# Performance work log

Measured on AMD Instinct MI355X. Metric: run time of the kernel, lower is better.

## Reference

```python
import jax, jax.numpy as jnp
import numpy as np

MAP_SIZE = 56
K_STEEP = 10.0  # boxcar sigmoid steepness (the 'k=10' default in the original)


def setup_inputs() -> dict:
    key = jax.random.key(0)
    k1, k2, k3 = jax.random.split(key, 3)
    B, D, H = 16384, 1024, 512
    x = jax.random.normal(k1, (B, D), dtype=jnp.float32)
    W1 = jax.random.normal(k2, (D, H), dtype=jnp.float32) * (1.0 / np.sqrt(D))
    b1 = jnp.zeros((H,), dtype=jnp.float32)
    W2 = jax.random.normal(k3, (H, 3), dtype=jnp.float32) * (1.0 / np.sqrt(H))
    b2 = jnp.zeros((3,), dtype=jnp.float32)
    return {"x": x, "W1": W1, "b1": b1, "W2": W2, "b2": b2}


def boxcar(t, map_size=MAP_SIZE, k=K_STEEP):
    # t: [B, 3] = (x_center, y_center, size). Vectorized over batch and grid.
    t0 = t[:, 0][:, None, None]  # [B,1,1]
    t1 = t[:, 1][:, None, None]
    t2 = t[:, 2][:, None, None]
    i = jnp.arange(map_size, dtype=t.dtype)[None, :, None]  # [1,S,1]
    j = jnp.arange(map_size, dtype=t.dtype)[None, None, :]  # [1,1,S]
    Vx = jax.nn.sigmoid(k * (i - t0 + 0.5 * t2)) - jax.nn.sigmoid(k * (i - t0 - 0.5 * t2))
    Vy = jax.nn.sigmoid(k * (j - t1 + 0.5 * t2)) - jax.nn.sigmoid(k * (j - t1 - 0.5 * t2))
    return Vx * Vy  # [B,S,S]


def reference(x, W1, b1, W2, b2):
    # fc1 -> fc2 (flatten output is discarded in the original call(), as in source)
    h = x @ W1 + b1          # [B, hidden]
    t = h @ W2 + b2          # [B, 3]
    return boxcar(t)         # [B, map_size, map_size]
```

## Files before the change

kernel.cpp:

```cpp
#include <hip/hip_runtime.h>
#include <math.h>

#define MAP 56
#define KST 10.0f
#define BATCH 16384
#define DIM 1024
#define HID 512
#define RPB 8

typedef float floatx4 __attribute__((ext_vector_type(4)));

__global__ __launch_bounds__(64) void fold_weights(
    const float* __restrict__ W1, const float* __restrict__ b1,
    const float* __restrict__ W2, const float* __restrict__ b2,
    float* __restrict__ WeffT, float* __restrict__ beff)
{
    const int d = blockIdx.x;
    const int lane = threadIdx.x;
    const float* row = (d < DIM) ? (W1 + (size_t)d * HID) : b1;

    float a0 = 0.f, a1 = 0.f, a2 = 0.f;
    for (int h = lane; h < HID; h += 64) {
        const float w = row[h];
        a0 += w * W2[h * 3 + 0];
        a1 += w * W2[h * 3 + 1];
        a2 += w * W2[h * 3 + 2];
    }
    #pragma unroll
    for (int off = 32; off; off >>= 1) {
        a0 += __shfl_down(a0, off, 64);
        a1 += __shfl_down(a1, off, 64);
        a2 += __shfl_down(a2, off, 64);
    }
    if (lane == 0) {
        if (d < DIM) {
            WeffT[0 * DIM + d] = a0;
            WeffT[1 * DIM + d] = a1;
            WeffT[2 * DIM + d] = a2;
        } else {
            beff[0] = a0 + b2[0];
            beff[1] = a1 + b2[1];
            beff[2] = a2 + b2[2];
        }
    }
}

__global__ __launch_bounds__(256) void fused_kernel(
    const float* __restrict__ x, const float* __restrict__ WeffT,
    const float* __restrict__ beff, float* __restrict__ out)
{
    __shared__ float   sVx[RPB][MAP];
    __shared__ floatx4 sVy4[RPB][MAP / 4];
    __shared__ float   st[RPB][4];

    const int tid  = threadIdx.x;
    const int wave = tid >> 6;
    const int lane = tid & 63;
    const int base = blockIdx.x * RPB;

    const float* xr0 = x + (size_t)(base + 2 * wave + 0) * DIM + 4 * lane;
    const float* xr1 = x + (size_t)(base + 2 * wave + 1) * DIM + 4 * lane;
    float a00 = 0.f, a01 = 0.f, a02 = 0.f;
    float a10 = 0.f, a11 = 0.f, a12 = 0.f;
    #pragma unroll
    for (int q = 0; q < 4; ++q) {
        const int off = 256 * q;
        const floatx4 w0 = *(const floatx4*)(WeffT + 0 * DIM + 4 * lane + off);
        const floatx4 w1 = *(const floatx4*)(WeffT + 1 * DIM + 4 * lane + off);
        const floatx4 w2 = *(const floatx4*)(WeffT + 2 * DIM + 4 * lane + off);
        const floatx4 x0 = __builtin_nontemporal_load((const floatx4*)(xr0 + off));
        const floatx4 x1 = __builtin_nontemporal_load((const floatx4*)(xr1 + off));
        a00 += x0.x * w0.x + x0.y * w0.y + x0.z * w0.z + x0.w * w0.w;
        a01 += x0.x * w1.x + x0.y * w1.y + x0.z * w1.z + x0.w * w1.w;
        a02 += x0.x * w2.x + x0.y * w2.y + x0.z * w2.z + x0.w * w2.w;
        a10 += x1.x * w0.x + x1.y * w0.y + x1.z * w0.z + x1.w * w0.w;
        a11 += x1.x * w1.x + x1.y * w1.y + x1.z * w1.z + x1.w * w1.w;
        a12 += x1.x * w2.x + x1.y * w2.y + x1.z * w2.z + x1.w * w2.w;
    }
    #pragma unroll
    for (int off = 32; off; off >>= 1) {
        a00 += __shfl_down(a00, off, 64);
        a01 += __shfl_down(a01, off, 64);
        a02 += __shfl_down(a02, off, 64);
        a10 += __shfl_down(a10, off, 64);
        a11 += __shfl_down(a11, off, 64);
        a12 += __shfl_down(a12, off, 64);
    }
    if (lane == 0) {
        const float b0 = beff[0], b1 = beff[1], b2 = beff[2];
        st[2 * wave + 0][0] = a00 + b0;
        st[2 * wave + 0][1] = a01 + b1;
        st[2 * wave + 0][2] = a02 + b2;
        st[2 * wave + 1][0] = a10 + b0;
        st[2 * wave + 1][1] = a11 + b1;
        st[2 * wave + 1][2] = a12 + b2;
    }
    __syncthreads();

    for (int e = tid; e < RPB * 2 * MAP; e += 256) {
        const int sub = e / (2 * MAP);
        const int ent = e - sub * (2 * MAP);
        const int isY = ent >= MAP;
        const int i   = isY ? ent - MAP : ent;
        const float tc = isY ? st[sub][1] : st[sub][0];
        const float u  = (float)i - tc;
        const float hh = 0.5f * st[sub][2];
        const float p  = 1.0f / (1.0f + __expf(-KST * (u + hh)));
        const float m  = 1.0f / (1.0f + __expf(-KST * (u - hh)));
        const float v  = p - m;
        if (isY) ((float*)&sVy4[sub][0])[i] = v;
        else     sVx[sub][i] = v;
    }
    __syncthreads();

    floatx4* ob = (floatx4*)(out + (size_t)base * (MAP * MAP));
    for (int g = tid; g < RPB * (MAP * MAP / 4); g += 256) {
        const int sub = g / (MAP * MAP / 4);
        const int rem = g - sub * (MAP * MAP / 4);
        const int i   = rem / (MAP / 4);
        const int jq  = rem - i * (MAP / 4);
        const float   vx = sVx[sub][i];
        const floatx4 vy = sVy4[sub][jq];
        floatx4 o;
        o.x = vx * vy.x; o.y = vx * vy.y; o.z = vx * vy.z; o.w = vx * vy.w;
        ob[g] = o;
    }
}

extern "C" void kernel_launch(void* const* d_in, const int* in_sizes, int n_in,
                              void* d_out, int out_size, void* d_ws, size_t ws_size,
                              hipStream_t stream) {
    const float* x  = (const float*)d_in[0];
    const float* W1 = (const float*)d_in[1];
    const float* b1 = (const float*)d_in[2];
    const float* W2 = (const float*)d_in[3];
    const float* b2 = (const float*)d_in[4];
    float* out = (float*)d_out;

    float* WeffT = (float*)d_ws;
    float* beff  = WeffT + 3 * DIM;

    fold_weights<<<DIM + 1, 64, 0, stream>>>(W1, b1, W2, b2, WeffT, beff);
    fused_kernel<<<BATCH / RPB, 256, 0, stream>>>(x, WeffT, beff, out);
}
```

Before: 264.4 us.

## Split fused kernel into separate GEMV and render kernels with per-wave rows

Splits the single fused kernel into a GEMV kernel, which writes the per-row (x, y, size) parameters to workspace, and a render kernel that produces the 56x56 boxcar maps. Each wave now handles one row independently, and the block-wide __syncthreads is replaced by a wave-local LDS wait, so the stages no longer stall each other inside a block. In exchange it adds a kernel launch and a small global round trip for the parameters. It also drops the nontemporal hint on the x loads.

```diff
diff --git a/kernel.cpp b/kernel.cpp
--- a/kernel.cpp
+++ b/kernel.cpp
@@ -6,7 +6,6 @@
 #define BATCH 16384
 #define DIM 1024
 #define HID 512
-#define RPB 8
 
 typedef float floatx4 __attribute__((ext_vector_type(4)));
 
@@ -45,82 +44,79 @@
     }
 }
 
-__global__ __launch_bounds__(256) void fused_kernel(
+__global__ __launch_bounds__(256) void gemv_kernel(
     const float* __restrict__ x, const float* __restrict__ WeffT,
-    const float* __restrict__ beff, float* __restrict__ out)
+    const float* __restrict__ beff, float* __restrict__ t4)
 {
-    __shared__ float   sVx[RPB][MAP];
-    __shared__ floatx4 sVy4[RPB][MAP / 4];
-    __shared__ float   st[RPB][4];
-
     const int tid  = threadIdx.x;
     const int wave = tid >> 6;
     const int lane = tid & 63;
-    const int base = blockIdx.x * RPB;
+    const int row  = blockIdx.x * 4 + wave;
 
-    const float* xr0 = x + (size_t)(base + 2 * wave + 0) * DIM + 4 * lane;
-    const float* xr1 = x + (size_t)(base + 2 * wave + 1) * DIM + 4 * lane;
-    float a00 = 0.f, a01 = 0.f, a02 = 0.f;
-    float a10 = 0.f, a11 = 0.f, a12 = 0.f;
+    const float* xr = x + (size_t)row * DIM + 4 * lane;
+    float a0 = 0.f, a1 = 0.f, a2 = 0.f;
     #pragma unroll
     for (int q = 0; q < 4; ++q) {
         const int off = 256 * q;
         const floatx4 w0 = *(const floatx4*)(WeffT + 0 * DIM + 4 * lane + off);
         const floatx4 w1 = *(const floatx4*)(WeffT + 1 * DIM + 4 * lane + off);
         const floatx4 w2 = *(const floatx4*)(WeffT + 2 * DIM + 4 * lane + off);
-        const floatx4 x0 = __builtin_nontemporal_load((const floatx4*)(xr0 + off));
-        const floatx4 x1 = __builtin_nontemporal_load((const floatx4*)(xr1 + off));
-        a00 += x0.x * w0.x + x0.y * w0.y + x0.z * w0.z + x0.w * w0.w;
-        a01 += x0.x * w1.x + x0.y * w1.y + x0.z * w1.z + x0.w * w1.w;
-        a02 += x0.x * w2.x + x0.y * w2.y + x0.z * w2.z + x0.w * w2.w;
-        a10 += x1.x * w0.x + x1.y * w0.y + x1.z * w0.z + x1.w * w0.w;
-        a11 += x1.x * w1.x + x1.y * w1.y + x1.z * w1.z + x1.w * w1.w;
-        a12 += x1.x * w2.x + x1.y * w2.y + x1.z * w2.z + x1.w * w2.w;
+        const floatx4 xv = *(const floatx4*)(xr + off);
+        a0 += xv.x * w0.x + xv.y * w0.y + xv.z * w0.z + xv.w * w0.w;
+        a1 += xv.x * w1.x + xv.y * w1.y + xv.z * w1.z + xv.w * w1.w;
+        a2 += xv.x * w2.x + xv.y * w2.y + xv.z * w2.z + xv.w * w2.w;
     }
     #pragma unroll
     for (int off = 32; off; off >>= 1) {
-        a00 += __shfl_down(a00, off, 64);
-        a01 += __shfl_down(a01, off, 64);
-        a02 += __shfl_down(a02, off, 64);
-        a10 += __shfl_down(a10, off, 64);
-        a11 += __shfl_down(a11, off, 64);
-        a12 += __shfl_down(a12, off, 64);
+        a0 += __shfl_down(a0, off, 64);
+        a1 += __shfl_down(a1, off, 64);
+        a2 += __shfl_down(a2, off, 64);
     }
     if (lane == 0) {
-        const float b0 = beff[0], b1 = beff[1], b2 = beff[2];
-        st[2 * wave + 0][0] = a00 + b0;
-        st[2 * wave + 0][1] = a01 + b1;
-        st[2 * wave + 0][2] = a02 + b2;
-        st[2 * wave + 1][0] = a10 + b0;
-        st[2 * wave + 1][1] = a11 + b1;
-        st[2 * wave + 1][2] = a12 + b2;
+        floatx4 o;
+        o.x = a0 + beff[0];
+        o.y = a1 + beff[1];
+        o.z = a2 + beff[2];
+        o.w = 0.f;
+        *(floatx4*)(t4 + (size_t)row * 4) = o;
     }
-    __syncthreads();
+}
 
-    for (int e = tid; e < RPB * 2 * MAP; e += 256) {
-        const int sub = e / (2 * MAP);
-        const int ent = e - sub * (2 * MAP);
-        const int isY = ent >= MAP;
-        const int i   = isY ? ent - MAP : ent;
-        const float tc = isY ? st[sub][1] : st[sub][0];
-        const float u  = (float)i - tc;
-        const float hh = 0.5f * st[sub][2];
-        const float p  = 1.0f / (1.0f + __expf(-KST * (u + hh)));
-        const float m  = 1.0f / (1.0f + __expf(-KST * (u - hh)));
-        const float v  = p - m;
-        if (isY) ((float*)&sVy4[sub][0])[i] = v;
-        else     sVx[sub][i] = v;
+__global__ __launch_bounds__(256) void render_kernel(
+    const float* __restrict__ t4, float* __restrict__ out)
+{
+    __shared__ float sV[4][128];
+
+    const int tid  = threadIdx.x;
+    const int wave = tid >> 6;
+    const int lane = tid & 63;
+    const int row  = blockIdx.x * 4 + wave;
+
+    const floatx4 tv = *(const floatx4*)(t4 + (size_t)row * 4);
+    const float hh = 0.5f * tv.z;
+
+    #pragma unroll
+    for (int p = 0; p < 2; ++p) {
+        const int e = lane + 64 * p;
+        if (e < 2 * MAP) {
+            const int   isY = e >= MAP;
+            const int   i   = isY ? e - MAP : e;
+            const float tc  = isY ? tv.y : tv.x;
+            const float u   = (float)i - tc;
+            const float pp  = 1.0f / (1.0f + __expf(-KST * (u + hh)));
+            const float mm  = 1.0f / (1.0f + __expf(-KST * (u - hh)));
+            sV[wave][(isY ? 64 : 0) + i] = pp - mm;
+        }
     }
-    __syncthreads();
+    asm volatile("s_waitcnt lgkmcnt(0)" ::: "memory");
 
-    floatx4* ob = (floatx4*)(out + (size_t)base * (MAP * MAP));
-    for (int g = tid; g < RPB * (MAP * MAP / 4); g += 256) {
-        const int sub = g / (MAP * MAP / 4);
-        const int rem = g - sub * (MAP * MAP / 4);
-        const int i   = rem / (MAP / 4);
-        const int jq  = rem - i * (MAP / 4);
-        const float   vx = sVx[sub][i];
-        const floatx4 vy = sVy4[sub][jq];
+    floatx4* ob = (floatx4*)(out + (size_t)row * (MAP * MAP));
+    const floatx4* vy4 = (const floatx4*)&sV[wave][64];
+    for (int g = lane; g < MAP * MAP / 4; g += 64) {
+        const int   i  = g / (MAP / 4);
+        const int   jq = g - i * (MAP / 4);
+        const float vx = sV[wave][i];
+        const floatx4 vy = vy4[jq];
         floatx4 o;
         o.x = vx * vy.x; o.y = vx * vy.y; o.z = vx * vy.z; o.w = vx * vy.w;
         ob[g] = o;
@@ -139,7 +135,9 @@
 
     float* WeffT = (float*)d_ws;
     float* beff  = WeffT + 3 * DIM;
+    float* t4    = beff + 4;
 
     fold_weights<<<DIM + 1, 64, 0, stream>>>(W1, b1, W2, b2, WeffT, beff);
-    fused_kernel<<<BATCH / RPB, 256, 0, stream>>>(x, WeffT, beff, out);
+    gemv_kernel<<<BATCH / 4, 256, 0, stream>>>(x, WeffT, beff, t4);
+    render_kernel<<<BATCH / 4, 256, 0, stream>>>(t4, out);
 }
```

Result: no change. 268.0 us (+1.3%).
